# Optimization experiments

Hardware: AMD Instinct MI355X
Metric: run time of the kernel (lower is better)

Reference implementation:

```python
import jax, jax.numpy as jnp
import numpy as np

N_NODES = 40000
N_EDGES = 640000
IN_DIM = 128
EDGE_DIM = 64
HID = 128


def setup_inputs() -> dict:
    key = jax.random.key(0)
    ks = jax.random.split(key, 12)
    s = 0.05  # small param scale keeps exp(attention) well-behaved
    return {
        "node_features": jax.random.normal(ks[0], (N_NODES, IN_DIM), jnp.float32),
        "edge_index": jax.random.randint(ks[1], (2, N_EDGES), 0, N_NODES, jnp.int32),
        "edge_features": jax.random.normal(ks[2], (N_EDGES, EDGE_DIM), jnp.float32),
        "W_node": jax.random.normal(ks[3], (IN_DIM, HID), jnp.float32) * s,
        "b_node": jnp.zeros((HID,), jnp.float32),
        "W_edge": jax.random.normal(ks[4], (EDGE_DIM, HID), jnp.float32) * s,
        "b_edge": jnp.zeros((HID,), jnp.float32),
        "W_att1": jax.random.normal(ks[5], (3 * HID, HID), jnp.float32) * s,
        "b_att1": jnp.zeros((HID,), jnp.float32),
        "W_att2": jax.random.normal(ks[6], (HID, 1), jnp.float32) * s,
        "b_att2": jnp.zeros((1,), jnp.float32),
        "W_out": jax.random.normal(ks[7], (HID, HID), jnp.float32) * s,
        "b_out": jnp.zeros((HID,), jnp.float32),
        "ln_gamma": jnp.ones((HID,), jnp.float32),
        "ln_beta": jnp.zeros((HID,), jnp.float32),
    }


def reference(node_features, edge_index, edge_features, W_node, b_node,
              W_edge, b_edge, W_att1, b_att1, W_att2, b_att2,
              W_out, b_out, ln_gamma, ln_beta):
    N = node_features.shape[0]
    src, dst = edge_index[0], edge_index[1]
    # per-edge-type node/edge transforms
    h = node_features @ W_node + b_node          # [N, H]
    he = edge_features @ W_edge + b_edge          # [E, H]
    h_src = h[src]                                # [E, H]
    h_dst = h[dst]                                # [E, H]
    cat = jnp.concatenate([h_src, h_dst, he], axis=1)  # [E, 3H]
    att = jnp.tanh(cat @ W_att1 + b_att1) @ W_att2 + b_att2  # [E, 1]
    # softmax over edges grouped by src (unstabilized exp, matching source)
    att_exp = jnp.exp(att)
    denom = jax.ops.segment_sum(att_exp, src, num_segments=N)  # [N, 1]
    coeff = att_exp / denom[src]                  # [E, 1]
    # weighted scatter-aggregate onto src nodes
    agg = jax.ops.segment_sum(h_dst * coeff, src, num_segments=N)  # [N, H]
    # output transform: Linear -> LayerNorm -> ReLU
    o = agg @ W_out + b_out
    mu = jnp.mean(o, axis=-1, keepdims=True)
    var = jnp.mean(jnp.square(o - mu), axis=-1, keepdims=True)
    o = (o - mu) * jax.lax.rsqrt(var + 1e-5) * ln_gamma + ln_beta
    return jax.nn.relu(o)
```

## Files before the change

### kernel.cpp

```cpp
#include <hip/hip_runtime.h>
#include <math.h>

#define N_NODES 40000
#define N_EDGES 640000
#define IN_DIM 128
#define EDGE_DIM 64
#define HID 128

typedef __attribute__((ext_vector_type(8))) short bf16x8;
typedef __attribute__((ext_vector_type(4))) float f32x4;

__device__ __forceinline__ ushort f2bf(float f) {
    unsigned int x = __float_as_uint(f);
    x += 0x7fffu + ((x >> 16) & 1u);
    return (ushort)(x >> 16);
}
__device__ __forceinline__ float bf2f(ushort u) {
    return __uint_as_float(((unsigned int)u) << 16);
}
__device__ __forceinline__ float tanh_fast(float x) {
    return 1.f - __fdividef(2.f, __expf(2.f * x) + 1.f);
}

__global__ __launch_bounds__(256) void k_wcomb(
    const float* __restrict__ W_edge, const float* __restrict__ W1,
    const float* __restrict__ b_att1, const float* __restrict__ b_edge,
    float* __restrict__ Wc, float* __restrict__ b_eff)
{
    const float* W1he = W1 + 256 * 128;
    if (blockIdx.x == 32) {
        const int n = threadIdx.x;
        if (n < 128) {
            float s = b_att1[n];
            for (int k = 0; k < 128; ++k) s = fmaf(b_edge[k], W1he[k * 128 + n], s);
            b_eff[n] = s;
        }
        return;
    }
    const int idx = blockIdx.x * 256 + threadIdx.x;
    const int row = idx >> 7, n = idx & 127;
    float s = 0.f;
    for (int k = 0; k < 128; ++k) s = fmaf(W_edge[row * 128 + k], W1he[k * 128 + n], s);
    Wc[idx] = s;
}

__global__ __launch_bounds__(256) void k_pack(
    const float* __restrict__ W1, const float* __restrict__ Wc,
    const float* __restrict__ Wn, const float* __restrict__ Wo,
    ushort* __restrict__ packB, ushort* __restrict__ packA,
    ushort* __restrict__ packN, ushort* __restrict__ packO)
{
    const int idx = blockIdx.x * 256 + threadIdx.x;
    if (idx < 32768) {
        const int j = idx & 7, lane = (idx >> 3) & 63, nt = (idx >> 9) & 7, k0 = idx >> 12;
        const int k = k0 * 32 + (lane >> 4) * 8 + j;
        const int n = nt * 16 + (lane & 15);
        packB[idx] = f2bf(W1[k * 128 + n]);
    } else if (idx < 40960) {
        const int i2 = idx - 32768;
        const int j = i2 & 7, lane = (i2 >> 3) & 63, mt = (i2 >> 9) & 7, k0 = i2 >> 12;
        const int k = k0 * 32 + (lane >> 4) * 8 + j;
        const int row = mt * 16 + (lane & 15);
        packA[i2] = f2bf(Wc[k * 128 + row]);
    } else if (idx < 57344) {
        const int i3 = idx - 40960;
        const int j = i3 & 7, lane = (i3 >> 3) & 63, nt = (i3 >> 9) & 7, k0 = i3 >> 12;
        const int k = k0 * 32 + (lane >> 4) * 8 + j;
        const int n = nt * 16 + (lane & 15);
        packN[i3] = f2bf(Wn[k * 128 + n]);
    } else {
        const int i4 = idx - 57344;
        const int j = i4 & 7, lane = (i4 >> 3) & 63, nt = (i4 >> 9) & 7, k0 = i4 >> 12;
        const int k = k0 * 32 + (lane >> 4) * 8 + j;
        const int n = nt * 16 + (lane & 15);
        packO[i4] = f2bf(Wo[k * 128 + n]);
    }
}

__global__ __launch_bounds__(256) void k_node_gemm(
    const float* __restrict__ X, const ushort* __restrict__ packN,
    const float* __restrict__ b, ushort* __restrict__ Hb)
{
    const int tid = threadIdx.x;
    const int wave = tid >> 6, lane = tid & 63;
    const int r = lane & 15, g = lane >> 4;
    const int nbase = blockIdx.x * 64 + wave * 16;
    const float* rowX = X + (size_t)(nbase + r) * 128 + g * 8;
    const bf16x8* Bp = reinterpret_cast<const bf16x8*>(packN);

    f32x4 acc[8];
#pragma unroll
    for (int nt = 0; nt < 8; ++nt) {
        const float bv = b[nt * 16 + r];
        acc[nt] = (f32x4){bv, bv, bv, bv};
    }
#pragma unroll
    for (int k0 = 0; k0 < 4; ++k0) {
        const float4 u0 = *reinterpret_cast<const float4*>(rowX + k0 * 32);
        const float4 u1 = *reinterpret_cast<const float4*>(rowX + k0 * 32 + 4);
        bf16x8 a;
        a[0] = (short)f2bf(u0.x); a[1] = (short)f2bf(u0.y);
        a[2] = (short)f2bf(u0.z); a[3] = (short)f2bf(u0.w);
        a[4] = (short)f2bf(u1.x); a[5] = (short)f2bf(u1.y);
        a[6] = (short)f2bf(u1.z); a[7] = (short)f2bf(u1.w);
#pragma unroll
        for (int nt = 0; nt < 8; ++nt)
            acc[nt] = __builtin_amdgcn_mfma_f32_16x16x32_bf16(
                a, Bp[(k0 * 8 + nt) * 64 + lane], acc[nt], 0, 0, 0);
    }
#pragma unroll
    for (int nt = 0; nt < 8; ++nt) {
#pragma unroll
        for (int q = 0; q < 4; ++q)
            Hb[(size_t)(nbase + g * 4 + q) * 128 + nt * 16 + r] = f2bf(acc[nt][q]);
    }
}

__global__ __launch_bounds__(256) void k_node_g12(
    const ushort* __restrict__ Hb, const ushort* __restrict__ packB,
    const float* __restrict__ b_eff,
    ushort* __restrict__ G1, ushort* __restrict__ G2)
{
    const int tid = threadIdx.x;
    const int wave = tid >> 6, lane = tid & 63;
    const int r = lane & 15, g = lane >> 4;
    const int nbase = blockIdx.x * 64 + wave * 16;
    const ushort* rowA = Hb + (size_t)(nbase + r) * 128 + g * 8;
    const bf16x8* Bp = reinterpret_cast<const bf16x8*>(packB);
    const int coff = (r >> 2) * 32 + (r & 3);

    f32x4 acc[8];
#pragma unroll
    for (int nt = 0; nt < 8; ++nt) acc[nt] = (f32x4){0.f, 0.f, 0.f, 0.f};
#pragma unroll
    for (int k0 = 0; k0 < 4; ++k0) {
        const bf16x8 a = *reinterpret_cast<const bf16x8*>(rowA + k0 * 32);
#pragma unroll
        for (int nt = 0; nt < 8; ++nt)
            acc[nt] = __builtin_amdgcn_mfma_f32_16x16x32_bf16(
                a, Bp[(k0 * 8 + nt) * 64 + lane], acc[nt], 0, 0, 0);
    }
#pragma unroll
    for (int nt = 0; nt < 8; ++nt) {
        const float bv = b_eff[nt * 16 + r];
#pragma unroll
        for (int q = 0; q < 4; ++q)
            G1[(size_t)(nbase + g * 4 + q) * 128 + coff + nt * 4] = f2bf(acc[nt][q] + bv);
    }

#pragma unroll
    for (int nt = 0; nt < 8; ++nt) acc[nt] = (f32x4){0.f, 0.f, 0.f, 0.f};
#pragma unroll
    for (int k0 = 0; k0 < 4; ++k0) {
        const bf16x8 a = *reinterpret_cast<const bf16x8*>(rowA + k0 * 32);
#pragma unroll
        for (int nt = 0; nt < 8; ++nt)
            acc[nt] = __builtin_amdgcn_mfma_f32_16x16x32_bf16(
                a, Bp[((k0 + 4) * 8 + nt) * 64 + lane], acc[nt], 0, 0, 0);
    }
#pragma unroll
    for (int nt = 0; nt < 8; ++nt) {
#pragma unroll
        for (int q = 0; q < 4; ++q)
            G2[(size_t)(nbase + g * 4 + q) * 128 + coff + nt * 4] = f2bf(acc[nt][q]);
    }
}

__global__ __launch_bounds__(256) void k_hist(
    const int* __restrict__ srcI, int* __restrict__ cnt)
{
    const int e = blockIdx.x * 256 + threadIdx.x;
    atomicAdd(&cnt[srcI[e]], 1);
}

__global__ __launch_bounds__(1024) void k_scan(
    const int* __restrict__ cnt, int* __restrict__ rowptr)
{
    __shared__ int wsum[16];
    __shared__ int carry;
    const int tid = threadIdx.x, lane = tid & 63, wid = tid >> 6;
    if (tid == 0) { carry = 0; rowptr[0] = 0; }
    __syncthreads();
    for (int base = 0; base < N_NODES; base += 4096) {
        const int i = base + tid * 4;
        int4 c = {0, 0, 0, 0};
        if (i < N_NODES) c = *reinterpret_cast<const int4*>(cnt + i);
        const int tsum = c.x + c.y + c.z + c.w;
        int v = tsum;
#pragma unroll
        for (int d = 1; d < 64; d <<= 1) {
            const int t = __shfl_up(v, d, 64);
            if (lane >= d) v += t;
        }
        if (lane == 63) wsum[wid] = v;
        __syncthreads();
        if (wid == 0 && lane < 16) {
            int w = wsum[lane];
#pragma unroll
            for (int d = 1; d < 16; d <<= 1) {
                const int t = __shfl_up(w, d, 16);
                if ((lane & 15) >= d) w += t;
            }
            wsum[lane] = w;
        }
        __syncthreads();
        const int off = (wid == 0) ? 0 : wsum[wid - 1];
        const int excl = carry + off + v - tsum;
        if (i < N_NODES) {
            rowptr[i + 1] = excl + c.x;
            rowptr[i + 2] = excl + c.x + c.y;
            rowptr[i + 3] = excl + c.x + c.y + c.z;
            rowptr[i + 4] = excl + tsum;
        }
        const int total = wsum[15];
        __syncthreads();
        if (tid == 0) carry += total;
        __syncthreads();
    }
}

__global__ __launch_bounds__(256) void k_fill(
    const int* __restrict__ srcI, const int* __restrict__ dstI,
    const int* __restrict__ rowptr, int* __restrict__ cursor,
    int2* __restrict__ edrec)
{
    const int e = blockIdx.x * 256 + threadIdx.x;
    const int s = srcI[e];
    const int pos = rowptr[s] + atomicAdd(&cursor[s], 1);
    int2 rec;
    rec.x = e;
    rec.y = (s << 16) | dstI[e];
    edrec[pos] = rec;
}

__global__ __launch_bounds__(256) void k_edge_att_v9(
    const int2* __restrict__ edrec, const float* __restrict__ EF,
    const ushort* __restrict__ G1, const ushort* __restrict__ G2,
    const ushort* __restrict__ packA,
    const float* __restrict__ W2, const float* __restrict__ b2,
    float* __restrict__ csr_p)
{
    const int tid = threadIdx.x;
    const int wave = tid >> 6, lane = tid & 63;
    const int r = lane & 15, g = lane >> 4;
    const int pbase = blockIdx.x * 64 + wave * 16;
    const int pos = pbase + r;
    const int2 rec = edrec[pos];
    const int e = rec.x;
    const int di = rec.y & 0xffff;
    const int si = ((unsigned)rec.y) >> 16;

    const ushort* g1base = G1 + (size_t)si * 128 + g * 32;
    const ushort* g2base = G2 + (size_t)di * 128 + g * 32;
    f32x4 acc[8];
#pragma unroll
    for (int mt2 = 0; mt2 < 4; ++mt2) {
        const bf16x8 a = *reinterpret_cast<const bf16x8*>(g1base + mt2 * 8);
        const bf16x8 c = *reinterpret_cast<const bf16x8*>(g2base + mt2 * 8);
#pragma unroll
        for (int q = 0; q < 4; ++q) {
            acc[2 * mt2][q]     = bf2f((ushort)a[q])     + bf2f((ushort)c[q]);
            acc[2 * mt2 + 1][q] = bf2f((ushort)a[4 + q]) + bf2f((ushort)c[4 + q]);
        }
    }

    const float* rowE = EF + (size_t)e * 64 + g * 8;
    bf16x8 b0, b1;
    {
        const float4 u0 = *reinterpret_cast<const float4*>(rowE);
        const float4 u1 = *reinterpret_cast<const float4*>(rowE + 4);
        b0[0] = (short)f2bf(u0.x); b0[1] = (short)f2bf(u0.y);
        b0[2] = (short)f2bf(u0.z); b0[3] = (short)f2bf(u0.w);
        b0[4] = (short)f2bf(u1.x); b0[5] = (short)f2bf(u1.y);
        b0[6] = (short)f2bf(u1.z); b0[7] = (short)f2bf(u1.w);
        const float4 v0 = *reinterpret_cast<const float4*>(rowE + 32);
        const float4 v1 = *reinterpret_cast<const float4*>(rowE + 36);
        b1[0] = (short)f2bf(v0.x); b1[1] = (short)f2bf(v0.y);
        b1[2] = (short)f2bf(v0.z); b1[3] = (short)f2bf(v0.w);
        b1[4] = (short)f2bf(v1.x); b1[5] = (short)f2bf(v1.y);
        b1[6] = (short)f2bf(v1.z); b1[7] = (short)f2bf(v1.w);
    }

    const bf16x8* Ap = reinterpret_cast<const bf16x8*>(packA);
#pragma unroll
    for (int mt = 0; mt < 8; ++mt)
        acc[mt] = __builtin_amdgcn_mfma_f32_16x16x32_bf16(
            Ap[(0 * 8 + mt) * 64 + lane], b0, acc[mt], 0, 0, 0);
#pragma unroll
    for (int mt = 0; mt < 8; ++mt)
        acc[mt] = __builtin_amdgcn_mfma_f32_16x16x32_bf16(
            Ap[(1 * 8 + mt) * 64 + lane], b1, acc[mt], 0, 0, 0);

    float part = 0.f;
#pragma unroll
    for (int mt = 0; mt < 8; ++mt) {
        const float4 w2v = *reinterpret_cast<const float4*>(W2 + mt * 16 + g * 4);
        part = fmaf(tanh_fast(acc[mt][0]), w2v.x, part);
        part = fmaf(tanh_fast(acc[mt][1]), w2v.y, part);
        part = fmaf(tanh_fast(acc[mt][2]), w2v.z, part);
        part = fmaf(tanh_fast(acc[mt][3]), w2v.w, part);
    }
    part += __shfl_xor(part, 16, 64);
    part += __shfl_xor(part, 32, 64);
    if (lane < 16) csr_p[pos] = __expf(part + b2[0]);
}

__global__ __launch_bounds__(256) void k_agg(
    const int* __restrict__ rowptr, const float* __restrict__ csr_p,
    const int2* __restrict__ edrec, const ushort* __restrict__ Hb,
    ushort* __restrict__ AGGb)
{
    const int tid = threadIdx.x;
    const int wave = tid >> 6, lane = tid & 63;
    const int slot = lane >> 4, tc = lane & 15;
    const int n = blockIdx.x * 4 + wave;
    const int beg = rowptr[n], end = rowptr[n + 1];

    float v[8];
#pragma unroll
    for (int i = 0; i < 8; ++i) v[i] = 0.f;
    float sp = 0.f;
    for (int j = beg + slot; j < end; j += 4) {
        const float p = csr_p[j];
        const int d = edrec[j].y & 0xffff;
        const bf16x8 hv = *reinterpret_cast<const bf16x8*>(Hb + (size_t)d * 128 + tc * 8);
#pragma unroll
        for (int i = 0; i < 8; ++i) v[i] = fmaf(p, bf2f((ushort)hv[i]), v[i]);
        sp += p;
    }
#pragma unroll
    for (int m = 16; m <= 32; m <<= 1) {
#pragma unroll
        for (int i = 0; i < 8; ++i) v[i] += __shfl_xor(v[i], m, 64);
        sp += __shfl_xor(sp, m, 64);
    }
    if (lane < 16) {
        const float inv = (end > beg) ? 1.f / sp : 0.f;
        bf16x8 o;
#pragma unroll
        for (int i = 0; i < 8; ++i) o[i] = (short)f2bf(v[i] * inv);
        *reinterpret_cast<bf16x8*>(AGGb + (size_t)n * 128 + tc * 8) = o;
    }
}

__global__ __launch_bounds__(256) void k_out_ln(
    const ushort* __restrict__ AGGb, const ushort* __restrict__ packO,
    const float* __restrict__ b, const float* __restrict__ gamma,
    const float* __restrict__ beta, float* __restrict__ OUT)
{
    const int tid = threadIdx.x;
    const int wave = tid >> 6, lane = tid & 63;
    const int r = lane & 15, g = lane >> 4;
    const int nbase = blockIdx.x * 64 + wave * 16;
    const ushort* rowA = AGGb + (size_t)(nbase + r) * 128 + g * 8;
    const bf16x8* Bp = reinterpret_cast<const bf16x8*>(packO);

    f32x4 acc[8];
#pragma unroll
    for (int nt = 0; nt < 8; ++nt) {
        const float bv = b[nt * 16 + r];
        acc[nt] = (f32x4){bv, bv, bv, bv};
    }
#pragma unroll
    for (int k0 = 0; k0 < 4; ++k0) {
        const bf16x8 a = *reinterpret_cast<const bf16x8*>(rowA + k0 * 32);
#pragma unroll
        for (int nt = 0; nt < 8; ++nt)
            acc[nt] = __builtin_amdgcn_mfma_f32_16x16x32_bf16(
                a, Bp[(k0 * 8 + nt) * 64 + lane], acc[nt], 0, 0, 0);
    }

    float s1[4] = {0.f, 0.f, 0.f, 0.f};
    float s2[4] = {0.f, 0.f, 0.f, 0.f};
#pragma unroll
    for (int nt = 0; nt < 8; ++nt) {
#pragma unroll
        for (int q = 0; q < 4; ++q) {
            const float z = acc[nt][q];
            s1[q] += z;
            s2[q] = fmaf(z, z, s2[q]);
        }
    }
#pragma unroll
    for (int m = 1; m <= 8; m <<= 1) {
#pragma unroll
        for (int q = 0; q < 4; ++q) {
            s1[q] += __shfl_xor(s1[q], m, 64);
            s2[q] += __shfl_xor(s2[q], m, 64);
        }
    }
    float mu[4], rr[4];
#pragma unroll
    for (int q = 0; q < 4; ++q) {
        mu[q] = s1[q] * (1.f / 128.f);
        const float var = s2[q] * (1.f / 128.f) - mu[q] * mu[q];
        rr[q] = rsqrtf(var + 1e-5f);
    }
#pragma unroll
    for (int nt = 0; nt < 8; ++nt) {
        const int col = nt * 16 + r;
        const float ga = gamma[col], be = beta[col];
#pragma unroll
        for (int q = 0; q < 4; ++q) {
            const float o = (acc[nt][q] - mu[q]) * rr[q] * ga + be;
            OUT[(size_t)(nbase + g * 4 + q) * 128 + col] = o > 0.f ? o : 0.f;
        }
    }
}

extern "C" void kernel_launch(void* const* d_in, const int* in_sizes, int n_in,
                              void* d_out, int out_size, void* d_ws, size_t ws_size,
                              hipStream_t stream)
{
    const float* node_features = (const float*)d_in[0];
    const int*   edge_index    = (const int*)d_in[1];
    const float* edge_features = (const float*)d_in[2];
    const float* W_node  = (const float*)d_in[3];
    const float* b_node  = (const float*)d_in[4];
    const float* W_edge  = (const float*)d_in[5];
    const float* b_edge  = (const float*)d_in[6];
    const float* W_att1  = (const float*)d_in[7];
    const float* b_att1  = (const float*)d_in[8];
    const float* W_att2  = (const float*)d_in[9];
    const float* b_att2  = (const float*)d_in[10];
    const float* W_out   = (const float*)d_in[11];
    const float* b_out   = (const float*)d_in[12];
    const float* ln_gamma = (const float*)d_in[13];
    const float* ln_beta  = (const float*)d_in[14];
    float* out = (float*)d_out;

    char* ws = (char*)d_ws;
    ushort* hb      = (ushort*)(ws);
    ushort* G1      = (ushort*)(ws + 10240000);
    ushort* G2      = (ushort*)(ws + 20480000);
    ushort* aggb    = (ushort*)(ws + 30720000);
    float*  csr_p   = (float*)(ws + 40960000);
    int2*   edrec   = (int2*)(ws + 43520000);
    int*    rowptr  = (int*)(ws + 48640000);
    int*    cnt     = (int*)(ws + 48800016);
    int*    cursor  = (int*)(ws + 48960016);
    float*  Wc      = (float*)(ws + 49120016);
    float*  b_eff   = (float*)(ws + 49152784);
    ushort* packB   = (ushort*)(ws + 49153296);
    ushort* packA   = (ushort*)(ws + 49218832);
    ushort* packN   = (ushort*)(ws + 49235216);
    ushort* packO   = (ushort*)(ws + 49267984);

    const int* srcI = edge_index;
    const int* dstI = edge_index + N_EDGES;

    hipMemsetAsync(cnt, 0, 320000, stream);

    k_wcomb<<<33, 256, 0, stream>>>(W_edge, W_att1, b_att1, b_edge, Wc, b_eff);
    k_pack<<<288, 256, 0, stream>>>(W_att1, Wc, W_node, W_out,
                                    packB, packA, packN, packO);
    k_node_gemm<<<N_NODES / 64, 256, 0, stream>>>(node_features, packN, b_node, hb);
    k_node_g12<<<N_NODES / 64, 256, 0, stream>>>(hb, packB, b_eff, G1, G2);
    k_hist<<<N_EDGES / 256, 256, 0, stream>>>(srcI, cnt);
    k_scan<<<1, 1024, 0, stream>>>(cnt, rowptr);
    k_fill<<<N_EDGES / 256, 256, 0, stream>>>(srcI, dstI, rowptr, cursor, edrec);
    k_edge_att_v9<<<N_EDGES / 64, 256, 0, stream>>>(edrec, edge_features,
                                                    G1, G2, packA, W_att2, b_att2,
                                                    csr_p);
    k_agg<<<N_NODES / 4, 256, 0, stream>>>(rowptr, csr_p, edrec, hb, aggb);
    k_out_ln<<<N_NODES / 64, 256, 0, stream>>>(aggb, packO, b_out, ln_gamma, ln_beta, out);
}
```

Baseline: 243.8 us.

## Merge independent setup kernels into combined launches and restructure edge/agg loops

```diff
diff --git a/kernel.cpp b/kernel.cpp
--- a/kernel.cpp
+++ b/kernel.cpp
@@ -22,160 +22,71 @@
     return 1.f - __fdividef(2.f, __expf(2.f * x) + 1.f);
 }
 
-__global__ __launch_bounds__(256) void k_wcomb(
+__global__ __launch_bounds__(256) void k_A(
     const float* __restrict__ W_edge, const float* __restrict__ W1,
     const float* __restrict__ b_att1, const float* __restrict__ b_edge,
-    float* __restrict__ Wc, float* __restrict__ b_eff)
-{
-    const float* W1he = W1 + 256 * 128;
-    if (blockIdx.x == 32) {
-        const int n = threadIdx.x;
-        if (n < 128) {
-            float s = b_att1[n];
-            for (int k = 0; k < 128; ++k) s = fmaf(b_edge[k], W1he[k * 128 + n], s);
-            b_eff[n] = s;
-        }
-        return;
-    }
-    const int idx = blockIdx.x * 256 + threadIdx.x;
-    const int row = idx >> 7, n = idx & 127;
-    float s = 0.f;
-    for (int k = 0; k < 128; ++k) s = fmaf(W_edge[row * 128 + k], W1he[k * 128 + n], s);
-    Wc[idx] = s;
-}
-
-__global__ __launch_bounds__(256) void k_pack(
+    float* __restrict__ Wc, float* __restrict__ b_eff,
+    const int* __restrict__ srcI, int* __restrict__ cnt)
+{
+    const int bid = blockIdx.x;
+    if (bid < 33) {
+        const float* W1he = W1 + 256 * 128;
+        if (bid == 32) {
+            const int n = threadIdx.x;
+            if (n < 128) {
+                float s = b_att1[n];
+                for (int k = 0; k < 128; ++k) s = fmaf(b_edge[k], W1he[k * 128 + n], s);
+                b_eff[n] = s;
+            }
+            return;
+        }
+        const int idx = bid * 256 + threadIdx.x;
+        const int row = idx >> 7, n = idx & 127;
+        float s = 0.f;
+        for (int k = 0; k < 128; ++k) s = fmaf(W_edge[row * 128 + k], W1he[k * 128 + n], s);
+        Wc[idx] = s;
+    } else {
+        const int e = (bid - 33) * 256 + threadIdx.x;
+        atomicAdd(&cnt[srcI[e]], 1);
+    }
+}
+
+__global__ __launch_bounds__(1024) void k_B(
     const float* __restrict__ W1, const float* __restrict__ Wc,
     const float* __restrict__ Wn, const float* __restrict__ Wo,
     ushort* __restrict__ packB, ushort* __restrict__ packA,
-    ushort* __restrict__ packN, ushort* __restrict__ packO)
-{
-    const int idx = blockIdx.x * 256 + threadIdx.x;
-    if (idx < 32768) {
-        const int j = idx & 7, lane = (idx >> 3) & 63, nt = (idx >> 9) & 7, k0 = idx >> 12;
-        const int k = k0 * 32 + (lane >> 4) * 8 + j;
-        const int n = nt * 16 + (lane & 15);
-        packB[idx] = f2bf(W1[k * 128 + n]);
-    } else if (idx < 40960) {
-        const int i2 = idx - 32768;
-        const int j = i2 & 7, lane = (i2 >> 3) & 63, mt = (i2 >> 9) & 7, k0 = i2 >> 12;
-        const int k = k0 * 32 + (lane >> 4) * 8 + j;
-        const int row = mt * 16 + (lane & 15);
-        packA[i2] = f2bf(Wc[k * 128 + row]);
-    } else if (idx < 57344) {
-        const int i3 = idx - 40960;
-        const int j = i3 & 7, lane = (i3 >> 3) & 63, nt = (i3 >> 9) & 7, k0 = i3 >> 12;
-        const int k = k0 * 32 + (lane >> 4) * 8 + j;
-        const int n = nt * 16 + (lane & 15);
-        packN[i3] = f2bf(Wn[k * 128 + n]);
-    } else {
-        const int i4 = idx - 57344;
-        const int j = i4 & 7, lane = (i4 >> 3) & 63, nt = (i4 >> 9) & 7, k0 = i4 >> 12;
-        const int k = k0 * 32 + (lane >> 4) * 8 + j;
-        const int n = nt * 16 + (lane & 15);
-        packO[i4] = f2bf(Wo[k * 128 + n]);
-    }
-}
-
-__global__ __launch_bounds__(256) void k_node_gemm(
-    const float* __restrict__ X, const ushort* __restrict__ packN,
-    const float* __restrict__ b, ushort* __restrict__ Hb)
-{
-    const int tid = threadIdx.x;
-    const int wave = tid >> 6, lane = tid & 63;
-    const int r = lane & 15, g = lane >> 4;
-    const int nbase = blockIdx.x * 64 + wave * 16;
-    const float* rowX = X + (size_t)(nbase + r) * 128 + g * 8;
-    const bf16x8* Bp = reinterpret_cast<const bf16x8*>(packN);
-
-    f32x4 acc[8];
-#pragma unroll
-    for (int nt = 0; nt < 8; ++nt) {
-        const float bv = b[nt * 16 + r];
-        acc[nt] = (f32x4){bv, bv, bv, bv};
-    }
-#pragma unroll
-    for (int k0 = 0; k0 < 4; ++k0) {
-        const float4 u0 = *reinterpret_cast<const float4*>(rowX + k0 * 32);
-        const float4 u1 = *reinterpret_cast<const float4*>(rowX + k0 * 32 + 4);
-        bf16x8 a;
-        a[0] = (short)f2bf(u0.x); a[1] = (short)f2bf(u0.y);
-        a[2] = (short)f2bf(u0.z); a[3] = (short)f2bf(u0.w);
-        a[4] = (short)f2bf(u1.x); a[5] = (short)f2bf(u1.y);
-        a[6] = (short)f2bf(u1.z); a[7] = (short)f2bf(u1.w);
-#pragma unroll
-        for (int nt = 0; nt < 8; ++nt)
-            acc[nt] = __builtin_amdgcn_mfma_f32_16x16x32_bf16(
-                a, Bp[(k0 * 8 + nt) * 64 + lane], acc[nt], 0, 0, 0);
-    }
-#pragma unroll
-    for (int nt = 0; nt < 8; ++nt) {
-#pragma unroll
-        for (int q = 0; q < 4; ++q)
-            Hb[(size_t)(nbase + g * 4 + q) * 128 + nt * 16 + r] = f2bf(acc[nt][q]);
-    }
-}
-
-__global__ __launch_bounds__(256) void k_node_g12(
-    const ushort* __restrict__ Hb, const ushort* __restrict__ packB,
-    const float* __restrict__ b_eff,
-    ushort* __restrict__ G1, ushort* __restrict__ G2)
-{
-    const int tid = threadIdx.x;
-    const int wave = tid >> 6, lane = tid & 63;
-    const int r = lane & 15, g = lane >> 4;
-    const int nbase = blockIdx.x * 64 + wave * 16;
-    const ushort* rowA = Hb + (size_t)(nbase + r) * 128 + g * 8;
-    const bf16x8* Bp = reinterpret_cast<const bf16x8*>(packB);
-    const int coff = (r >> 2) * 32 + (r & 3);
-
-    f32x4 acc[8];
-#pragma unroll
-    for (int nt = 0; nt < 8; ++nt) acc[nt] = (f32x4){0.f, 0.f, 0.f, 0.f};
-#pragma unroll
-    for (int k0 = 0; k0 < 4; ++k0) {
-        const bf16x8 a = *reinterpret_cast<const bf16x8*>(rowA + k0 * 32);
-#pragma unroll
-        for (int nt = 0; nt < 8; ++nt)
-            acc[nt] = __builtin_amdgcn_mfma_f32_16x16x32_bf16(
-                a, Bp[(k0 * 8 + nt) * 64 + lane], acc[nt], 0, 0, 0);
-    }
-#pragma unroll
-    for (int nt = 0; nt < 8; ++nt) {
-        const float bv = b_eff[nt * 16 + r];
-#pragma unroll
-        for (int q = 0; q < 4; ++q)
-            G1[(size_t)(nbase + g * 4 + q) * 128 + coff + nt * 4] = f2bf(acc[nt][q] + bv);
-    }
-
-#pragma unroll
-    for (int nt = 0; nt < 8; ++nt) acc[nt] = (f32x4){0.f, 0.f, 0.f, 0.f};
-#pragma unroll
-    for (int k0 = 0; k0 < 4; ++k0) {
-        const bf16x8 a = *reinterpret_cast<const bf16x8*>(rowA + k0 * 32);
-#pragma unroll
-        for (int nt = 0; nt < 8; ++nt)
-            acc[nt] = __builtin_amdgcn_mfma_f32_16x16x32_bf16(
-                a, Bp[((k0 + 4) * 8 + nt) * 64 + lane], acc[nt], 0, 0, 0);
-    }
-#pragma unroll
-    for (int nt = 0; nt < 8; ++nt) {
-#pragma unroll
-        for (int q = 0; q < 4; ++q)
-            G2[(size_t)(nbase + g * 4 + q) * 128 + coff + nt * 4] = f2bf(acc[nt][q]);
-    }
-}
-
-__global__ __launch_bounds__(256) void k_hist(
-    const int* __restrict__ srcI, int* __restrict__ cnt)
-{
-    const int e = blockIdx.x * 256 + threadIdx.x;
-    atomicAdd(&cnt[srcI[e]], 1);
-}
-
-__global__ __launch_bounds__(1024) void k_scan(
+    ushort* __restrict__ packN, ushort* __restrict__ packO,
     const int* __restrict__ cnt, int* __restrict__ rowptr)
 {
+    const int bid = blockIdx.x;
+    if (bid < 72) {
+        const int idx = bid * 1024 + threadIdx.x;
+        if (idx < 32768) {
+            const int j = idx & 7, lane = (idx >> 3) & 63, nt = (idx >> 9) & 7, k0 = idx >> 12;
+            const int k = k0 * 32 + (lane >> 4) * 8 + j;
+            const int n = nt * 16 + (lane & 15);
+            packB[idx] = f2bf(W1[k * 128 + n]);
+        } else if (idx < 40960) {
+            const int i2 = idx - 32768;
+            const int j = i2 & 7, lane = (i2 >> 3) & 63, mt = (i2 >> 9) & 7, k0 = i2 >> 12;
+            const int k = k0 * 32 + (lane >> 4) * 8 + j;
+            const int row = mt * 16 + (lane & 15);
+            packA[i2] = f2bf(Wc[k * 128 + row]);
+        } else if (idx < 57344) {
+            const int i3 = idx - 40960;
+            const int j = i3 & 7, lane = (i3 >> 3) & 63, nt = (i3 >> 9) & 7, k0 = i3 >> 12;
+            const int k = k0 * 32 + (lane >> 4) * 8 + j;
+            const int n = nt * 16 + (lane & 15);
+            packN[i3] = f2bf(Wn[k * 128 + n]);
+        } else {
+            const int i4 = idx - 57344;
+            const int j = i4 & 7, lane = (i4 >> 3) & 63, nt = (i4 >> 9) & 7, k0 = i4 >> 12;
+            const int k = k0 * 32 + (lane >> 4) * 8 + j;
+            const int n = nt * 16 + (lane & 15);
+            packO[i4] = f2bf(Wo[k * 128 + n]);
+        }
+        return;
+    }
     __shared__ int wsum[16];
     __shared__ int carry;
     const int tid = threadIdx.x, lane = tid & 63, wid = tid >> 6;
@@ -219,21 +130,110 @@
     }
 }
 
-__global__ __launch_bounds__(256) void k_fill(
+__global__ __launch_bounds__(256) void k_C(
+    const float* __restrict__ X, const ushort* __restrict__ packN,
+    const float* __restrict__ b, ushort* __restrict__ Hb,
     const int* __restrict__ srcI, const int* __restrict__ dstI,
     const int* __restrict__ rowptr, int* __restrict__ cursor,
     int2* __restrict__ edrec)
 {
-    const int e = blockIdx.x * 256 + threadIdx.x;
-    const int s = srcI[e];
-    const int pos = rowptr[s] + atomicAdd(&cursor[s], 1);
-    int2 rec;
-    rec.x = e;
-    rec.y = (s << 16) | dstI[e];
-    edrec[pos] = rec;
-}
-
-__global__ __launch_bounds__(256) void k_edge_att_v9(
+    const int bid = blockIdx.x;
+    if (bid >= 625) {
+        const int e = (bid - 625) * 256 + threadIdx.x;
+        const int s = srcI[e];
+        const int pos = rowptr[s] + atomicAdd(&cursor[s], 1);
+        int2 rec;
+        rec.x = e;
+        rec.y = (s << 16) | dstI[e];
+        edrec[pos] = rec;
+        return;
+    }
+    const int tid = threadIdx.x;
+    const int wave = tid >> 6, lane = tid & 63;
+    const int r = lane & 15, g = lane >> 4;
+    const int nbase = bid * 64 + wave * 16;
+    const float* rowX = X + (size_t)(nbase + r) * 128 + g * 8;
+    const bf16x8* Bp = reinterpret_cast<const bf16x8*>(packN);
+
+    f32x4 acc[8];
+#pragma unroll
+    for (int nt = 0; nt < 8; ++nt) {
+        const float bv = b[nt * 16 + r];
+        acc[nt] = (f32x4){bv, bv, bv, bv};
+    }
+#pragma unroll
+    for (int k0 = 0; k0 < 4; ++k0) {
+        const float4 u0 = *reinterpret_cast<const float4*>(rowX + k0 * 32);
+        const float4 u1 = *reinterpret_cast<const float4*>(rowX + k0 * 32 + 4);
+        bf16x8 a;
+        a[0] = (short)f2bf(u0.x); a[1] = (short)f2bf(u0.y);
+        a[2] = (short)f2bf(u0.z); a[3] = (short)f2bf(u0.w);
+        a[4] = (short)f2bf(u1.x); a[5] = (short)f2bf(u1.y);
+        a[6] = (short)f2bf(u1.z); a[7] = (short)f2bf(u1.w);
+#pragma unroll
+        for (int nt = 0; nt < 8; ++nt)
+            acc[nt] = __builtin_amdgcn_mfma_f32_16x16x32_bf16(
+                a, Bp[(k0 * 8 + nt) * 64 + lane], acc[nt], 0, 0, 0);
+    }
+#pragma unroll
+    for (int nt = 0; nt < 8; ++nt) {
+#pragma unroll
+        for (int q = 0; q < 4; ++q)
+            Hb[(size_t)(nbase + g * 4 + q) * 128 + nt * 16 + r] = f2bf(acc[nt][q]);
+    }
+}
+
+__global__ __launch_bounds__(256) void k_node_g12(
+    const ushort* __restrict__ Hb, const ushort* __restrict__ packB,
+    const float* __restrict__ b_eff,
+    ushort* __restrict__ G1, ushort* __restrict__ G2)
+{
+    const int tid = threadIdx.x;
+    const int wave = tid >> 6, lane = tid & 63;
+    const int r = lane & 15, g = lane >> 4;
+    const int nbase = blockIdx.x * 64 + wave * 16;
+    const ushort* rowA = Hb + (size_t)(nbase + r) * 128 + g * 8;
+    const bf16x8* Bp = reinterpret_cast<const bf16x8*>(packB);
+    const int coff = (r >> 2) * 32 + (r & 3);
+
+    f32x4 acc[8];
+#pragma unroll
+    for (int nt = 0; nt < 8; ++nt) acc[nt] = (f32x4){0.f, 0.f, 0.f, 0.f};
+#pragma unroll
+    for (int k0 = 0; k0 < 4; ++k0) {
+        const bf16x8 a = *reinterpret_cast<const bf16x8*>(rowA + k0 * 32);
+#pragma unroll
+        for (int nt = 0; nt < 8; ++nt)
+            acc[nt] = __builtin_amdgcn_mfma_f32_16x16x32_bf16(
+                a, Bp[(k0 * 8 + nt) * 64 + lane], acc[nt], 0, 0, 0);
+    }
+#pragma unroll
+    for (int nt = 0; nt < 8; ++nt) {
+        const float bv = b_eff[nt * 16 + r];
+#pragma unroll
+        for (int q = 0; q < 4; ++q)
+            G1[(size_t)(nbase + g * 4 + q) * 128 + coff + nt * 4] = f2bf(acc[nt][q] + bv);
+    }
+
+#pragma unroll
+    for (int nt = 0; nt < 8; ++nt) acc[nt] = (f32x4){0.f, 0.f, 0.f, 0.f};
+#pragma unroll
+    for (int k0 = 0; k0 < 4; ++k0) {
+        const bf16x8 a = *reinterpret_cast<const bf16x8*>(rowA + k0 * 32);
+#pragma unroll
+        for (int nt = 0; nt < 8; ++nt)
+            acc[nt] = __builtin_amdgcn_mfma_f32_16x16x32_bf16(
+                a, Bp[((k0 + 4) * 8 + nt) * 64 + lane], acc[nt], 0, 0, 0);
+    }
+#pragma unroll
+    for (int nt = 0; nt < 8; ++nt) {
+#pragma unroll
+        for (int q = 0; q < 4; ++q)
+            G2[(size_t)(nbase + g * 4 + q) * 128 + coff + nt * 4] = f2bf(acc[nt][q]);
+    }
+}
+
+__global__ __launch_bounds__(256) void k_edge_att_v10(
     const int2* __restrict__ edrec, const float* __restrict__ EF,
     const ushort* __restrict__ G1, const ushort* __restrict__ G2,
     const ushort* __restrict__ packA,
@@ -250,17 +250,21 @@
     const int di = rec.y & 0xffff;
     const int si = ((unsigned)rec.y) >> 16;
 
+    const ushort* g2base = G2 + (size_t)di * 128 + g * 32;
+    bf16x8 g2r[4];
+#pragma unroll
+    for (int m2 = 0; m2 < 4; ++m2)
+        g2r[m2] = *reinterpret_cast<const bf16x8*>(g2base + m2 * 8);
+
     const ushort* g1base = G1 + (size_t)si * 128 + g * 32;
-    const ushort* g2base = G2 + (size_t)di * 128 + g * 32;
     f32x4 acc[8];
 #pragma unroll
-    for (int mt2 = 0; mt2 < 4; ++mt2) {
-        const bf16x8 a = *reinterpret_cast<const bf16x8*>(g1base + mt2 * 8);
-        const bf16x8 c = *reinterpret_cast<const bf16x8*>(g2base + mt2 * 8);
+    for (int m2 = 0; m2 < 4; ++m2) {
+        const bf16x8 a = *reinterpret_cast<const bf16x8*>(g1base + m2 * 8);
 #pragma unroll
         for (int q = 0; q < 4; ++q) {
-            acc[2 * mt2][q]     = bf2f((ushort)a[q])     + bf2f((ushort)c[q]);
-            acc[2 * mt2 + 1][q] = bf2f((ushort)a[4 + q]) + bf2f((ushort)c[4 + q]);
+            acc[2 * m2][q]     = bf2f((ushort)a[q]);
+            acc[2 * m2 + 1][q] = bf2f((ushort)a[4 + q]);
         }
     }
 
@@ -294,11 +298,17 @@
     float part = 0.f;
 #pragma unroll
     for (int mt = 0; mt < 8; ++mt) {
+        const bf16x8 gr = g2r[mt >> 1];
+        const int h4 = (mt & 1) * 4;
         const float4 w2v = *reinterpret_cast<const float4*>(W2 + mt * 16 + g * 4);
-        part = fmaf(tanh_fast(acc[mt][0]), w2v.x, part);
-        part = fmaf(tanh_fast(acc[mt][1]), w2v.y, part);
-        part = fmaf(tanh_fast(acc[mt][2]), w2v.z, part);
-        part = fmaf(tanh_fast(acc[mt][3]), w2v.w, part);
+        const float z0 = acc[mt][0] + bf2f((ushort)gr[h4 + 0]);
+        const float z1 = acc[mt][1] + bf2f((ushort)gr[h4 + 1]);
+        const float z2 = acc[mt][2] + bf2f((ushort)gr[h4 + 2]);
+        const float z3 = acc[mt][3] + bf2f((ushort)gr[h4 + 3]);
+        part = fmaf(tanh_fast(z0), w2v.x, part);
+        part = fmaf(tanh_fast(z1), w2v.y, part);
+        part = fmaf(tanh_fast(z2), w2v.z, part);
+        part = fmaf(tanh_fast(z3), w2v.w, part);
     }
     part += __shfl_xor(part, 16, 64);
     part += __shfl_xor(part, 32, 64);
@@ -320,7 +330,23 @@
 #pragma unroll
     for (int i = 0; i < 8; ++i) v[i] = 0.f;
     float sp = 0.f;
-    for (int j = beg + slot; j < end; j += 4) {
+
+    int j = beg + slot;
+    for (; j + 4 < end; j += 8) {
+        const float p0 = csr_p[j];
+        const int d0 = edrec[j].y & 0xffff;
+        const float p1 = csr_p[j + 4];
+        const int d1 = edrec[j + 4].y & 0xffff;
+        const bf16x8 h0 = *reinterpret_cast<const bf16x8*>(Hb + (size_t)d0 * 128 + tc * 8);
+        const bf16x8 h1 = *reinterpret_cast<const bf16x8*>(Hb + (size_t)d1 * 128 + tc * 8);
+#pragma unroll
+        for (int i = 0; i < 8; ++i) {
+            v[i] = fmaf(p0, bf2f((ushort)h0[i]), v[i]);
+            v[i] = fmaf(p1, bf2f((ushort)h1[i]), v[i]);
+        }
+        sp += p0 + p1;
+    }
+    for (; j < end; j += 4) {
         const float p = csr_p[j];
         const int d = edrec[j].y & 0xffff;
         const bf16x8 hv = *reinterpret_cast<const bf16x8*>(Hb + (size_t)d * 128 + tc * 8);
@@ -451,17 +477,16 @@
 
     hipMemsetAsync(cnt, 0, 320000, stream);
 
-    k_wcomb<<<33, 256, 0, stream>>>(W_edge, W_att1, b_att1, b_edge, Wc, b_eff);
-    k_pack<<<288, 256, 0, stream>>>(W_att1, Wc, W_node, W_out,
-                                    packB, packA, packN, packO);
-    k_node_gemm<<<N_NODES / 64, 256, 0, stream>>>(node_features, packN, b_node, hb);
+    k_A<<<2533, 256, 0, stream>>>(W_edge, W_att1, b_att1, b_edge, Wc, b_eff,
+                                  srcI, cnt);
+    k_B<<<73, 1024, 0, stream>>>(W_att1, Wc, W_node, W_out,
+                                 packB, packA, packN, packO, cnt, rowptr);
+    k_C<<<3125, 256, 0, stream>>>(node_features, packN, b_node, hb,
+                                  srcI, dstI, rowptr, cursor, edrec);
     k_node_g12<<<N_NODES / 64, 256, 0, stream>>>(hb, packB, b_eff, G1, G2);
-    k_hist<<<N_EDGES / 256, 256, 0, stream>>>(srcI, cnt);
-    k_scan<<<1, 1024, 0, stream>>>(cnt, rowptr);
-    k_fill<<<N_EDGES / 256, 256, 0, stream>>>(srcI, dstI, rowptr, cursor, edrec);
-    k_edge_att_v9<<<N_EDGES / 64, 256, 0, stream>>>(edrec, edge_features,
-                                                    G1, G2, packA, W_att2, b_att2,
-                                                    csr_p);
+    k_edge_att_v10<<<N_EDGES / 64, 256, 0, stream>>>(edrec, edge_features,
+                                                     G1, G2, packA, W_att2, b_att2,
+                                                     csr_p);
     k_agg<<<N_NODES / 4, 256, 0, stream>>>(rowptr, csr_p, edrec, hb, aggb);
     k_out_ln<<<N_NODES / 64, 256, 0, stream>>>(aggb, packO, b_out, ln_gamma, ln_beta, out);
 }
```

New measurement: 231.2 us. -5.2%, faster.
